# Performance work log

Hardware: AMD Instinct MI355X
Metric: run time of the kernel (lower is better)

Reference implementation:

```python
import jax, jax.numpy as jnp
import numpy as np

N_LAYERS = 2
K_NEIGHBOURS = 30  # graph_top_K keeps k_neighbours + 1 entries per row
EPS = 1e-12        # torch F.normalize eps


def setup_inputs() -> dict:
    key = jax.random.key(0)
    k1, k2 = jax.random.split(key)
    N, d = 8192, 512
    x = jax.random.normal(k1, (N, d), dtype=jnp.float32)
    W = jax.random.normal(k2, (N_LAYERS, d, d), dtype=jnp.float32) * 0.02
    b = jnp.zeros((N_LAYERS, d), dtype=jnp.float32)
    return {"x": x, "W": W, "b": b}


def reference(x, W, b):
    # MLP: interval_forward -- relu between layers, linear on last layer
    h = x
    for i in range(N_LAYERS - 1):
        h = jax.nn.relu(h @ W[i].T + b[i])
    h = h @ W[N_LAYERS - 1].T + b[N_LAYERS - 1]

    # F.normalize(h, dim=-1, p=2)
    norm = jnp.linalg.norm(h, axis=-1, keepdims=True)
    h = h / jnp.maximum(norm, EPS)

    # cal_similarity_graph: dense N x N cosine similarity
    sim = h @ h.T  # [N, N]

    # graph_top_K(sim, k+1): keep top-(k+1) values per row, zero elsewhere
    k = K_NEIGHBOURS + 1
    vals, idx = jax.lax.top_k(sim, k)  # [N, k]
    N = sim.shape[0]
    masked = jnp.zeros_like(sim).at[jnp.arange(N)[:, None], idx].set(vals)

    # apply_non_linearity(x, 'relu', slope, alpha) -> relu
    return jax.nn.relu(masked)
```

## Files before the change

### kernel.cpp

```cpp
#include <hip/hip_runtime.h>
#include <hip/hip_bf16.h>

typedef __attribute__((ext_vector_type(8))) short bf16x8;
typedef __attribute__((ext_vector_type(8))) unsigned short u16x8;
typedef __attribute__((ext_vector_type(4))) float f32x4;

__global__ __launch_bounds__(256)
void gemm_nt(const float* __restrict__ A, const float* __restrict__ B,
             const float* __restrict__ bias, float* __restrict__ C,
             int M, int N, int K, int do_relu)
{
    constexpr int KS = 16;
    constexpr int LDT = 132;
    __shared__ float As[KS * LDT];
    __shared__ float Bs[KS * LDT];

    const int t    = threadIdx.x;
    const int row0 = blockIdx.y * 128;
    const int col0 = blockIdx.x * 128;
    const int tm   = t & 15;
    const int tn   = t >> 4;
    const int lrow = t >> 2;
    const int lk   = (t & 3) << 2;

    const float* Ap0 = A + (size_t)(row0 + lrow)      * K + lk;
    const float* Ap1 = A + (size_t)(row0 + lrow + 64) * K + lk;
    const float* Bp0 = B + (size_t)(col0 + lrow)      * K + lk;
    const float* Bp1 = B + (size_t)(col0 + lrow + 64) * K + lk;

    float4 a0 = *(const float4*)(Ap0);
    float4 a1 = *(const float4*)(Ap1);
    float4 b0 = *(const float4*)(Bp0);
    float4 b1 = *(const float4*)(Bp1);

    float acc[8][8];
#pragma unroll
    for (int i = 0; i < 8; ++i)
#pragma unroll
        for (int j = 0; j < 8; ++j) acc[i][j] = 0.f;

    for (int k0 = 0; k0 < K; k0 += KS) {
        __syncthreads();
        As[(lk + 0) * LDT + lrow] = a0.x;
        As[(lk + 1) * LDT + lrow] = a0.y;
        As[(lk + 2) * LDT + lrow] = a0.z;
        As[(lk + 3) * LDT + lrow] = a0.w;
        As[(lk + 0) * LDT + lrow + 64] = a1.x;
        As[(lk + 1) * LDT + lrow + 64] = a1.y;
        As[(lk + 2) * LDT + lrow + 64] = a1.z;
        As[(lk + 3) * LDT + lrow + 64] = a1.w;
        Bs[(lk + 0) * LDT + lrow] = b0.x;
        Bs[(lk + 1) * LDT + lrow] = b0.y;
        Bs[(lk + 2) * LDT + lrow] = b0.z;
        Bs[(lk + 3) * LDT + lrow] = b0.w;
        Bs[(lk + 0) * LDT + lrow + 64] = b1.x;
        Bs[(lk + 1) * LDT + lrow + 64] = b1.y;
        Bs[(lk + 2) * LDT + lrow + 64] = b1.z;
        Bs[(lk + 3) * LDT + lrow + 64] = b1.w;
        __syncthreads();
        if (k0 + KS < K) {
            a0 = *(const float4*)(Ap0 + k0 + KS);
            a1 = *(const float4*)(Ap1 + k0 + KS);
            b0 = *(const float4*)(Bp0 + k0 + KS);
            b1 = *(const float4*)(Bp1 + k0 + KS);
        }
#pragma unroll
        for (int kk = 0; kk < KS; ++kk) {
            const float4 av0 = *(const float4*)&As[kk * LDT + 8 * tm];
            const float4 av1 = *(const float4*)&As[kk * LDT + 8 * tm + 4];
            const float4 bv0 = *(const float4*)&Bs[kk * LDT + 8 * tn];
            const float4 bv1 = *(const float4*)&Bs[kk * LDT + 8 * tn + 4];
            const float a[8] = {av0.x, av0.y, av0.z, av0.w, av1.x, av1.y, av1.z, av1.w};
            const float bb[8] = {bv0.x, bv0.y, bv0.z, bv0.w, bv1.x, bv1.y, bv1.z, bv1.w};
#pragma unroll
            for (int i = 0; i < 8; ++i)
#pragma unroll
                for (int j = 0; j < 8; ++j)
                    acc[i][j] += a[i] * bb[j];
        }
    }

#pragma unroll
    for (int i = 0; i < 8; ++i) {
        const int r = row0 + 8 * tm + i;
        float* Crow = C + (size_t)r * N + col0 + 8 * tn;
        float o[8];
#pragma unroll
        for (int j = 0; j < 8; ++j) o[j] = acc[i][j];
        if (bias) {
#pragma unroll
            for (int j = 0; j < 8; ++j) o[j] += bias[col0 + 8 * tn + j];
        }
        if (do_relu) {
#pragma unroll
            for (int j = 0; j < 8; ++j) o[j] = fmaxf(o[j], 0.f);
        }
        float4 o0 = {o[0], o[1], o[2], o[3]};
        float4 o1 = {o[4], o[5], o[6], o[7]};
        *(float4*)(Crow)     = o0;
        *(float4*)(Crow + 4) = o1;
    }
}

__global__ __launch_bounds__(128)
void rownorm_split(const float* __restrict__ in, unsigned short* __restrict__ Hhi,
                   unsigned short* __restrict__ Hmid, unsigned short* __restrict__ Hlo)
{
    __shared__ float s[2];
    const int r = blockIdx.x, t = threadIdx.x;
    const float4 v = ((const float4*)(in + (size_t)r * 512))[t];
    float ss = v.x * v.x + v.y * v.y + v.z * v.z + v.w * v.w;
#pragma unroll
    for (int off = 32; off; off >>= 1) ss += __shfl_down(ss, off);
    if ((t & 63) == 0) s[t >> 6] = ss;
    __syncthreads();
    const float den = fmaxf(sqrtf(s[0] + s[1]), 1e-12f);
    const float f[4] = {v.x / den, v.y / den, v.z / den, v.w / den};
    ushort4 uh, um, ul;
    unsigned short* ph = (unsigned short*)&uh;
    unsigned short* pm = (unsigned short*)&um;
    unsigned short* pl = (unsigned short*)&ul;
#pragma unroll
    for (int j = 0; j < 4; ++j) {
        const __hip_bfloat16 h = __float2bfloat16(f[j]);
        const float fh = __bfloat162float(h);
        const float r1 = f[j] - fh;
        const __hip_bfloat16 m = __float2bfloat16(r1);
        const float fm = __bfloat162float(m);
        const float r2 = r1 - fm;
        const __hip_bfloat16 l = __float2bfloat16(r2);
        ph[j] = *(const unsigned short*)&h;
        pm[j] = *(const unsigned short*)&m;
        pl[j] = *(const unsigned short*)&l;
    }
    const size_t o = (size_t)r * 512 + 4 * t;
    *(ushort4*)(Hhi  + o) = uh;
    *(ushort4*)(Hmid + o) = um;
    *(ushort4*)(Hlo  + o) = ul;
}

__global__ __launch_bounds__(256)
void gemm_sym_mfma(const unsigned short* __restrict__ Hhi,
                   const unsigned short* __restrict__ Hmid,
                   const unsigned short* __restrict__ Hlo,
                   float* __restrict__ C, int Nn)
{
    constexpr int K  = 512;
    constexpr int KC = 32;
    constexpr int LR = 40;
    __shared__ unsigned short lds[6 * 128 * LR];

    const int q = blockIdx.x;
    int ct = (int)((sqrtf(8.0f * (float)q + 1.0f) - 1.0f) * 0.5f);
    while ((ct + 1) * (ct + 2) / 2 <= q) ++ct;
    while (ct * (ct + 1) / 2 > q) --ct;
    const int rt = q - ct * (ct + 1) / 2;
    const int row0 = rt * 128;
    const int col0 = ct * 128;

    const int t    = threadIdx.x;
    const int lane = t & 63;
    const int wid  = t >> 6;
    const int wr   = (wid >> 1) * 64;
    const int wc   = (wid & 1) * 64;

    const int r  = t >> 1;
    const int kh = (t & 1) * 16;
    const unsigned short* srcs[6] = {
        Hhi  + (size_t)(row0 + r) * K, Hmid + (size_t)(row0 + r) * K, Hlo + (size_t)(row0 + r) * K,
        Hhi  + (size_t)(col0 + r) * K, Hmid + (size_t)(col0 + r) * K, Hlo + (size_t)(col0 + r) * K };

    u16x8 pf[12];
#pragma unroll
    for (int a = 0; a < 6; ++a) {
        pf[2 * a]     = *(const u16x8*)(srcs[a] + kh);
        pf[2 * a + 1] = *(const u16x8*)(srcs[a] + kh + 8);
    }

    f32x4 acc[4][4];
#pragma unroll
    for (int i = 0; i < 4; ++i)
#pragma unroll
        for (int j = 0; j < 4; ++j) acc[i][j] = (f32x4){0.f, 0.f, 0.f, 0.f};

    const int fro = (lane & 15) * LR + 8 * (lane >> 4);

    for (int k0 = 0; k0 < K; k0 += KC) {
        __syncthreads();
#pragma unroll
        for (int a = 0; a < 6; ++a) {
            *(u16x8*)&lds[a * 128 * LR + r * LR + kh]     = pf[2 * a];
            *(u16x8*)&lds[a * 128 * LR + r * LR + kh + 8] = pf[2 * a + 1];
        }
        __syncthreads();
        if (k0 + KC < K) {
#pragma unroll
            for (int a = 0; a < 6; ++a) {
                pf[2 * a]     = *(const u16x8*)(srcs[a] + k0 + KC + kh);
                pf[2 * a + 1] = *(const u16x8*)(srcs[a] + k0 + KC + kh + 8);
            }
        }
        bf16x8 af[3][4], bf[3][4];
#pragma unroll
        for (int p = 0; p < 3; ++p)
#pragma unroll
            for (int ti = 0; ti < 4; ++ti) {
                af[p][ti] = *(const bf16x8*)&lds[p * 128 * LR + (wr + ti * 16) * LR + fro];
                bf[p][ti] = *(const bf16x8*)&lds[(3 + p) * 128 * LR + (wc + ti * 16) * LR + fro];
            }
#pragma unroll
        for (int ti = 0; ti < 4; ++ti)
#pragma unroll
            for (int tj = 0; tj < 4; ++tj) {
                f32x4 c = acc[ti][tj];
                c = __builtin_amdgcn_mfma_f32_16x16x32_bf16(af[0][ti], bf[0][tj], c, 0, 0, 0);
                c = __builtin_amdgcn_mfma_f32_16x16x32_bf16(af[0][ti], bf[1][tj], c, 0, 0, 0);
                c = __builtin_amdgcn_mfma_f32_16x16x32_bf16(af[1][ti], bf[0][tj], c, 0, 0, 0);
                c = __builtin_amdgcn_mfma_f32_16x16x32_bf16(af[1][ti], bf[1][tj], c, 0, 0, 0);
                c = __builtin_amdgcn_mfma_f32_16x16x32_bf16(af[0][ti], bf[2][tj], c, 0, 0, 0);
                c = __builtin_amdgcn_mfma_f32_16x16x32_bf16(af[2][ti], bf[0][tj], c, 0, 0, 0);
                acc[ti][tj] = c;
            }
    }

    const int crow = (lane >> 4) * 4;
    const int ccol = lane & 15;
#pragma unroll
    for (int ti = 0; ti < 4; ++ti)
#pragma unroll
        for (int tj = 0; tj < 4; ++tj)
#pragma unroll
            for (int qq = 0; qq < 4; ++qq) {
                const int rr = row0 + wr + ti * 16 + crow + qq;
                const int cc = col0 + wc + tj * 16 + ccol;
                C[(size_t)rr * Nn + cc] = acc[ti][tj][qq];
            }
    if (ct != rt) {
#pragma unroll
        for (int ti = 0; ti < 4; ++ti)
#pragma unroll
            for (int tj = 0; tj < 4; ++tj)
#pragma unroll
                for (int qq = 0; qq < 4; ++qq) {
                    const int rr = row0 + wr + ti * 16 + crow + qq;
                    const int cc = col0 + wc + tj * 16 + ccol;
                    C[(size_t)cc * Nn + rr] = acc[ti][tj][qq];
                }
    }
}

__global__ __launch_bounds__(128)
void rownorm(const float* __restrict__ in, float* __restrict__ out)
{
    __shared__ float s[2];
    const int r = blockIdx.x, t = threadIdx.x;
    const float4 v = ((const float4*)(in + (size_t)r * 512))[t];
    float ss = v.x * v.x + v.y * v.y + v.z * v.z + v.w * v.w;
#pragma unroll
    for (int off = 32; off; off >>= 1) ss += __shfl_down(ss, off);
    if ((t & 63) == 0) s[t >> 6] = ss;
    __syncthreads();
    const float den = fmaxf(sqrtf(s[0] + s[1]), 1e-12f);
    float4 o;
    o.x = v.x / den; o.y = v.y / den; o.z = v.z / den; o.w = v.w / den;
    ((float4*)(out + (size_t)r * 512))[t] = o;
}

__global__ __launch_bounds__(256)
void gemm_syn(const float* __restrict__ H, float* __restrict__ C, int Nn, int K)
{
    constexpr int KS = 16;
    constexpr int LDT = 132;
    __shared__ float As[KS * LDT];
    __shared__ float Bs[KS * LDT];

    const int q = blockIdx.x;
    int ct = (int)((sqrtf(8.0f * (float)q + 1.0f) - 1.0f) * 0.5f);
    while ((ct + 1) * (ct + 2) / 2 <= q) ++ct;
    while (ct * (ct + 1) / 2 > q) --ct;
    const int rt = q - ct * (ct + 1) / 2;
    const int row0 = rt * 128;
    const int col0 = ct * 128;

    const int t    = threadIdx.x;
    const int tm   = t & 15;
    const int tn   = t >> 4;
    const int lrow = t >> 2;
    const int lk   = (t & 3) << 2;

    const float* Ap0 = H + (size_t)(row0 + lrow)      * K + lk;
    const float* Ap1 = H + (size_t)(row0 + lrow + 64) * K + lk;
    const float* Bp0 = H + (size_t)(col0 + lrow)      * K + lk;
    const float* Bp1 = H + (size_t)(col0 + lrow + 64) * K + lk;

    float4 a0 = *(const float4*)(Ap0);
    float4 a1 = *(const float4*)(Ap1);
    float4 b0 = *(const float4*)(Bp0);
    float4 b1 = *(const float4*)(Bp1);

    float acc[8][8];
#pragma unroll
    for (int i = 0; i < 8; ++i)
#pragma unroll
        for (int j = 0; j < 8; ++j) acc[i][j] = 0.f;

    for (int k0 = 0; k0 < K; k0 += KS) {
        __syncthreads();
        As[(lk + 0) * LDT + lrow] = a0.x;
        As[(lk + 1) * LDT + lrow] = a0.y;
        As[(lk + 2) * LDT + lrow] = a0.z;
        As[(lk + 3) * LDT + lrow] = a0.w;
        As[(lk + 0) * LDT + lrow + 64] = a1.x;
        As[(lk + 1) * LDT + lrow + 64] = a1.y;
        As[(lk + 2) * LDT + lrow + 64] = a1.z;
        As[(lk + 3) * LDT + lrow + 64] = a1.w;
        Bs[(lk + 0) * LDT + lrow] = b0.x;
        Bs[(lk + 1) * LDT + lrow] = b0.y;
        Bs[(lk + 2) * LDT + lrow] = b0.z;
        Bs[(lk + 3) * LDT + lrow] = b0.w;
        Bs[(lk + 0) * LDT + lrow + 64] = b1.x;
        Bs[(lk + 1) * LDT + lrow + 64] = b1.y;
        Bs[(lk + 2) * LDT + lrow + 64] = b1.z;
        Bs[(lk + 3) * LDT + lrow + 64] = b1.w;
        __syncthreads();
        if (k0 + KS < K) {
            a0 = *(const float4*)(Ap0 + k0 + KS);
            a1 = *(const float4*)(Ap1 + k0 + KS);
            b0 = *(const float4*)(Bp0 + k0 + KS);
            b1 = *(const float4*)(Bp1 + k0 + KS);
        }
#pragma unroll
        for (int kk = 0; kk < KS; ++kk) {
            const float4 av0 = *(const float4*)&As[kk * LDT + 4 * tm];
            const float4 av1 = *(const float4*)&As[kk * LDT + 4 * tm + 64];
            const float4 bv0 = *(const float4*)&Bs[kk * LDT + 4 * tn];
            const float4 bv1 = *(const float4*)&Bs[kk * LDT + 4 * tn + 64];
            const float a[8] = {av0.x, av0.y, av0.z, av0.w, av1.x, av1.y, av1.z, av1.w};
            const float bb[8] = {bv0.x, bv0.y, bv0.z, bv0.w, bv1.x, bv1.y, bv1.z, bv1.w};
#pragma unroll
            for (int i = 0; i < 8; ++i)
#pragma unroll
                for (int j = 0; j < 8; ++j)
                    acc[i][j] += a[i] * bb[j];
        }
    }

#pragma unroll
    for (int ih = 0; ih < 2; ++ih)
#pragma unroll
    for (int i2 = 0; i2 < 4; ++i2) {
        const int rr = row0 + ih * 64 + 4 * tm + i2;
        float* Crow = C + (size_t)rr * Nn + col0;
        const int ia = ih * 4 + i2;
        float4 o0 = {acc[ia][0], acc[ia][1], acc[ia][2], acc[ia][3]};
        float4 o1 = {acc[ia][4], acc[ia][5], acc[ia][6], acc[ia][7]};
        *(float4*)(Crow + 4 * tn)      = o0;
        *(float4*)(Crow + 64 + 4 * tn) = o1;
    }
    if (ct != rt) {
#pragma unroll
        for (int jh = 0; jh < 2; ++jh)
#pragma unroll
        for (int j2 = 0; j2 < 4; ++j2) {
            const int rr = col0 + jh * 64 + 4 * tn + j2;
            float* Crow = C + (size_t)rr * Nn + row0;
            const int ja = jh * 4 + j2;
            float4 o0 = {acc[0][ja], acc[1][ja], acc[2][ja], acc[3][ja]};
            float4 o1 = {acc[4][ja], acc[5][ja], acc[6][ja], acc[7][ja]};
            *(float4*)(Crow + 4 * tm)      = o0;
            *(float4*)(Crow + 64 + 4 * tm) = o1;
        }
    }
}

__device__ __forceinline__ unsigned monou(unsigned b)
{
    return (b & 0x80000000u) ? ~b : (b | 0x80000000u);
}
__device__ __forceinline__ float unmono(unsigned u)
{
    return __uint_as_float((u & 0x80000000u) ? (u ^ 0x80000000u) : ~u);
}

__global__ __launch_bounds__(256)
void topk_bits(float* __restrict__ sim)
{
    constexpr int NC = 8192;
    constexpr unsigned KSEL = 31;
    __shared__ unsigned wsum[2][4];
    __shared__ int tie_idx[256];
    __shared__ int tie_cnt, sh_thr;

    const int t = threadIdx.x;
    const int lane = t & 63;
    const int wid = t >> 6;
    float* row = sim + (size_t)blockIdx.x * NC;

    if (t == 0) tie_cnt = 0;

    unsigned k[8][4];
#pragma unroll
    for (int j = 0; j < 8; ++j) {
        const uint4 v = *(const uint4*)&row[4 * (t + 256 * j)];
        k[j][0] = monou(v.x); k[j][1] = monou(v.y);
        k[j][2] = monou(v.z); k[j][3] = monou(v.w);
    }

    unsigned X = 0u;
    for (int b = 31; b >= 0; --b) {
        const unsigned cand = X | (1u << b);
        unsigned c = 0;
#pragma unroll
        for (int j = 0; j < 8; ++j)
#pragma unroll
            for (int e = 0; e < 4; ++e)
                c += (k[j][e] >= cand) ? 1u : 0u;
#pragma unroll
        for (int off = 32; off; off >>= 1) c += __shfl_xor(c, off);
        if (lane == 0) wsum[b & 1][wid] = c;
        __syncthreads();
        const unsigned tot = wsum[b & 1][0] + wsum[b & 1][1]
                           + wsum[b & 1][2] + wsum[b & 1][3];
        if (tot >= KSEL) X = cand;
    }
    const unsigned uc = X;

    {
        unsigned c = 0;
#pragma unroll
        for (int j = 0; j < 8; ++j)
#pragma unroll
            for (int e = 0; e < 4; ++e)
                c += (k[j][e] > uc) ? 1u : 0u;
#pragma unroll
        for (int off = 32; off; off >>= 1) c += __shfl_xor(c, off);
        if (lane == 0) wsum[1][wid] = c;
        __syncthreads();
    }
    const int m = (int)(KSEL - (wsum[1][0] + wsum[1][1] + wsum[1][2] + wsum[1][3]));

#pragma unroll
    for (int j = 0; j < 8; ++j)
#pragma unroll
        for (int e = 0; e < 4; ++e)
            if (k[j][e] == uc) {
                const int p = atomicAdd(&tie_cnt, 1);
                if (p < 256) tie_idx[p] = 4 * (t + 256 * j) + e;
            }
    __syncthreads();
    if (t == 0) {
        int n = tie_cnt < 256 ? tie_cnt : 256;
        for (int a = 1; a < n; ++a) {
            const int key = tie_idx[a];
            int c = a - 1;
            while (c >= 0 && tie_idx[c] > key) { tie_idx[c + 1] = tie_idx[c]; --c; }
            tie_idx[c + 1] = key;
        }
        const int mm = (m <= n ? m : n);
        sh_thr = tie_idx[mm - 1];
    }
    __syncthreads();
    const int tie_thr = sh_thr;

#pragma unroll
    for (int j = 0; j < 8; ++j) {
        const int i0 = 4 * (t + 256 * j);
        float4 v;
        v.x = (k[j][0] > uc || (k[j][0] == uc && i0 + 0 <= tie_thr)) ? fmaxf(unmono(k[j][0]), 0.f) : 0.f;
        v.y = (k[j][1] > uc || (k[j][1] == uc && i0 + 1 <= tie_thr)) ? fmaxf(unmono(k[j][1]), 0.f) : 0.f;
        v.z = (k[j][2] > uc || (k[j][2] == uc && i0 + 2 <= tie_thr)) ? fmaxf(unmono(k[j][2]), 0.f) : 0.f;
        v.w = (k[j][3] > uc || (k[j][3] == uc && i0 + 3 <= tie_thr)) ? fmaxf(unmono(k[j][3]), 0.f) : 0.f;
        *(float4*)&row[i0] = v;
    }
}

extern "C" void kernel_launch(void* const* d_in, const int* in_sizes, int n_in,
                              void* d_out, int out_size, void* d_ws, size_t ws_size,
                              hipStream_t stream)
{
    const float* x = (const float*)d_in[0];
    const float* W = (const float*)d_in[1];
    const float* b = (const float*)d_in[2];
    float* out = (float*)d_out;

    const int N = 8192, D = 512;
    const int T = N / 128;

    float* h1 = out;
    float* h2 = out + (size_t)N * D;

    dim3 tb(256);
    gemm_nt<<<dim3(D / 128, N / 128), tb, 0, stream>>>(x,  W,                 b,     h1, N, D, D, 1);
    gemm_nt<<<dim3(D / 128, N / 128), tb, 0, stream>>>(h1, W + (size_t)D * D, b + D, h2, N, D, D, 0);

    const size_t split_bytes = (size_t)3 * N * D * sizeof(unsigned short);
    if (ws_size >= split_bytes) {
        unsigned short* Hhi  = (unsigned short*)d_ws;
        unsigned short* Hmid = Hhi  + (size_t)N * D;
        unsigned short* Hlo  = Hmid + (size_t)N * D;
        rownorm_split<<<N, 128, 0, stream>>>(h2, Hhi, Hmid, Hlo);
        gemm_sym_mfma<<<T * (T + 1) / 2, tb, 0, stream>>>(Hhi, Hmid, Hlo, out, N);
    } else {
        float* hn = (float*)d_ws;
        rownorm<<<N, 128, 0, stream>>>(h2, hn);
        gemm_syn<<<T * (T + 1) / 2, tb, 0, stream>>>(hn, out, N, D);
    }
    topk_bits<<<N, tb, 0, stream>>>(out);
}
```

Measured before the change: 758.3 us.

## Shrink MLP GEMM tiles, swizzle MFMA LDS layout, and remap symmetric tile order

The MLP GEMMs move from 128x128 to 128x64 output tiles, doubling the block count to 512 so more CUs are busy, with a conflict-free strided thread mapping. In the symmetric bf16-split MFMA GEMM, the padded LDS rows are replaced by an XOR-swizzled 64-byte row layout to avoid bank conflicts without padding. Block indices are also permuted in an interleaved order (q0&7)*260+(q0>>3), which spreads triangular tiles across the GPU. Smaller MLP tiles lower per-block reuse, and the remap assumes exactly 2080 blocks.

After: 753.9 us. About the same (-0.6%).

```diff
diff --git a/kernel.cpp b/kernel.cpp
--- a/kernel.cpp
+++ b/kernel.cpp
@@ -6,27 +6,294 @@
 typedef __attribute__((ext_vector_type(4))) float f32x4;
 
 __global__ __launch_bounds__(256)
-void gemm_nt(const float* __restrict__ A, const float* __restrict__ B,
-             const float* __restrict__ bias, float* __restrict__ C,
-             int M, int N, int K, int do_relu)
+void gemm_nt64(const float* __restrict__ A, const float* __restrict__ B,
+               const float* __restrict__ bias, float* __restrict__ C,
+               int M, int N, int K, int do_relu)
+{
+    constexpr int KS = 16;
+    constexpr int LDA = 132;
+    constexpr int LDB = 68;
+    __shared__ float As[KS * LDA];
+    __shared__ float Bs[KS * LDB];
+
+    const int t    = threadIdx.x;
+    const int row0 = blockIdx.y * 128;
+    const int col0 = blockIdx.x * 64;
+    const int tm   = t & 15;
+    const int tn   = t >> 4;
+
+    const int arow = t >> 1;
+    const int ak   = (t & 1) * 8;
+    const int brow = t >> 2;
+    const int bk   = (t & 3) * 4;
+
+    const float* Ap = A + (size_t)(row0 + arow) * K + ak;
+    const float* Bp = B + (size_t)(col0 + brow) * K + bk;
+
+    float4 a0 = *(const float4*)(Ap);
+    float4 a1 = *(const float4*)(Ap + 4);
+    float4 b0 = *(const float4*)(Bp);
+
+    float acc[8][4];
+#pragma unroll
+    for (int i = 0; i < 8; ++i)
+#pragma unroll
+        for (int j = 0; j < 4; ++j) acc[i][j] = 0.f;
+
+    for (int k0 = 0; k0 < K; k0 += KS) {
+        __syncthreads();
+        As[(ak + 0) * LDA + arow] = a0.x;
+        As[(ak + 1) * LDA + arow] = a0.y;
+        As[(ak + 2) * LDA + arow] = a0.z;
+        As[(ak + 3) * LDA + arow] = a0.w;
+        As[(ak + 4) * LDA + arow] = a1.x;
+        As[(ak + 5) * LDA + arow] = a1.y;
+        As[(ak + 6) * LDA + arow] = a1.z;
+        As[(ak + 7) * LDA + arow] = a1.w;
+        Bs[(bk + 0) * LDB + brow] = b0.x;
+        Bs[(bk + 1) * LDB + brow] = b0.y;
+        Bs[(bk + 2) * LDB + brow] = b0.z;
+        Bs[(bk + 3) * LDB + brow] = b0.w;
+        __syncthreads();
+        if (k0 + KS < K) {
+            a0 = *(const float4*)(Ap + k0 + KS);
+            a1 = *(const float4*)(Ap + k0 + KS + 4);
+            b0 = *(const float4*)(Bp + k0 + KS);
+        }
+#pragma unroll
+        for (int kk = 0; kk < KS; ++kk) {
+            const float4 av0 = *(const float4*)&As[kk * LDA + 4 * tm];
+            const float4 av1 = *(const float4*)&As[kk * LDA + 64 + 4 * tm];
+            const float4 bv  = *(const float4*)&Bs[kk * LDB + 4 * tn];
+            const float a[8] = {av0.x, av0.y, av0.z, av0.w, av1.x, av1.y, av1.z, av1.w};
+            const float bb[4] = {bv.x, bv.y, bv.z, bv.w};
+#pragma unroll
+            for (int i = 0; i < 8; ++i)
+#pragma unroll
+                for (int j = 0; j < 4; ++j)
+                    acc[i][j] += a[i] * bb[j];
+        }
+    }
+
+#pragma unroll
+    for (int ih = 0; ih < 2; ++ih)
+#pragma unroll
+    for (int i2 = 0; i2 < 4; ++i2) {
+        const int r  = row0 + ih * 64 + 4 * tm + i2;
+        const int ia = ih * 4 + i2;
+        float o[4];
+#pragma unroll
+        for (int j = 0; j < 4; ++j) o[j] = acc[ia][j];
+        if (bias) {
+#pragma unroll
+            for (int j = 0; j < 4; ++j) o[j] += bias[col0 + 4 * tn + j];
+        }
+        if (do_relu) {
+#pragma unroll
+            for (int j = 0; j < 4; ++j) o[j] = fmaxf(o[j], 0.f);
+        }
+        float4 ov = {o[0], o[1], o[2], o[3]};
+        *(float4*)(C + (size_t)r * N + col0 + 4 * tn) = ov;
+    }
+}
+
+__global__ __launch_bounds__(128)
+void rownorm_split(const float* __restrict__ in, unsigned short* __restrict__ Hhi,
+                   unsigned short* __restrict__ Hmid, unsigned short* __restrict__ Hlo)
+{
+    __shared__ float s[2];
+    const int r = blockIdx.x, t = threadIdx.x;
+    const float4 v = ((const float4*)(in + (size_t)r * 512))[t];
+    float ss = v.x * v.x + v.y * v.y + v.z * v.z + v.w * v.w;
+#pragma unroll
+    for (int off = 32; off; off >>= 1) ss += __shfl_down(ss, off);
+    if ((t & 63) == 0) s[t >> 6] = ss;
+    __syncthreads();
+    const float den = fmaxf(sqrtf(s[0] + s[1]), 1e-12f);
+    const float f[4] = {v.x / den, v.y / den, v.z / den, v.w / den};
+    ushort4 uh, um, ul;
+    unsigned short* ph = (unsigned short*)&uh;
+    unsigned short* pm = (unsigned short*)&um;
+    unsigned short* pl = (unsigned short*)&ul;
+#pragma unroll
+    for (int j = 0; j < 4; ++j) {
+        const __hip_bfloat16 h = __float2bfloat16(f[j]);
+        const float fh = __bfloat162float(h);
+        const float r1 = f[j] - fh;
+        const __hip_bfloat16 m = __float2bfloat16(r1);
+        const float fm = __bfloat162float(m);
+        const float r2 = r1 - fm;
+        const __hip_bfloat16 l = __float2bfloat16(r2);
+        ph[j] = *(const unsigned short*)&h;
+        pm[j] = *(const unsigned short*)&m;
+        pl[j] = *(const unsigned short*)&l;
+    }
+    const size_t o = (size_t)r * 512 + 4 * t;
+    *(ushort4*)(Hhi  + o) = uh;
+    *(ushort4*)(Hmid + o) = um;
+    *(ushort4*)(Hlo  + o) = ul;
+}
+
+__global__ __launch_bounds__(256)
+void gemm_sym_mfma(const unsigned short* __restrict__ Hhi,
+                   const unsigned short* __restrict__ Hmid,
+                   const unsigned short* __restrict__ Hlo,
+                   float* __restrict__ C, int Nn)
+{
+    constexpr int K  = 512;
+    constexpr int KC = 32;
+    __shared__ unsigned short lds[6 * 128 * 32];
+
+    const int q0 = blockIdx.x;
+    const int q  = (q0 & 7) * 260 + (q0 >> 3);
+    int ct = (int)((sqrtf(8.0f * (float)q + 1.0f) - 1.0f) * 0.5f);
+    while ((ct + 1) * (ct + 2) / 2 <= q) ++ct;
+    while (ct * (ct + 1) / 2 > q) --ct;
+    const int rt = q - ct * (ct + 1) / 2;
+    const int row0 = rt * 128;
+    const int col0 = ct * 128;
+
+    const int t    = threadIdx.x;
+    const int lane = t & 63;
+    const int wid  = t >> 6;
+    const int wr   = (wid >> 1) * 64;
+    const int wc   = (wid & 1) * 64;
+
+    const int r   = t >> 1;
+    const int kh  = (t & 1) * 16;
+    const int wb  = r * 64 + kh * 2;
+    const int swW = ((r & 7) << 4);
+    const unsigned short* srcs[6] = {
+        Hhi  + (size_t)(row0 + r) * K, Hmid + (size_t)(row0 + r) * K, Hlo + (size_t)(row0 + r) * K,
+        Hhi  + (size_t)(col0 + r) * K, Hmid + (size_t)(col0 + r) * K, Hlo + (size_t)(col0 + r) * K };
+
+    u16x8 pf[12];
+#pragma unroll
+    for (int a = 0; a < 6; ++a) {
+        pf[2 * a]     = *(const u16x8*)(srcs[a] + kh);
+        pf[2 * a + 1] = *(const u16x8*)(srcs[a] + kh + 8);
+    }
+
+    f32x4 acc[4][4];
+#pragma unroll
+    for (int i = 0; i < 4; ++i)
+#pragma unroll
+        for (int j = 0; j < 4; ++j) acc[i][j] = (f32x4){0.f, 0.f, 0.f, 0.f};
+
+    const int g16 = (lane >> 4) << 4;
+    const int swR = ((lane & 7) << 4);
+    char* ldsb = (char*)lds;
+
+    for (int k0 = 0; k0 < K; k0 += KC) {
+        __syncthreads();
+#pragma unroll
+        for (int a = 0; a < 6; ++a) {
+            const int base = a * 8192 + wb;
+            *(u16x8*)(ldsb + ((base)      ^ swW)) = pf[2 * a];
+            *(u16x8*)(ldsb + ((base + 16) ^ swW)) = pf[2 * a + 1];
+        }
+        __syncthreads();
+        if (k0 + KC < K) {
+#pragma unroll
+            for (int a = 0; a < 6; ++a) {
+                pf[2 * a]     = *(const u16x8*)(srcs[a] + k0 + KC + kh);
+                pf[2 * a + 1] = *(const u16x8*)(srcs[a] + k0 + KC + kh + 8);
+            }
+        }
+        bf16x8 af[3][4], bf[3][4];
+#pragma unroll
+        for (int p = 0; p < 3; ++p)
+#pragma unroll
+            for (int ti = 0; ti < 4; ++ti) {
+                const int rA = wr + ti * 16 + (lane & 15);
+                const int rB = wc + ti * 16 + (lane & 15);
+                af[p][ti] = *(const bf16x8*)(ldsb + ((p * 8192 + rA * 64 + g16) ^ swR));
+                bf[p][ti] = *(const bf16x8*)(ldsb + (((3 + p) * 8192 + rB * 64 + g16) ^ swR));
+            }
+#pragma unroll
+        for (int ti = 0; ti < 4; ++ti)
+#pragma unroll
+            for (int tj = 0; tj < 4; ++tj) {
+                f32x4 c = acc[ti][tj];
+                c = __builtin_amdgcn_mfma_f32_16x16x32_bf16(af[0][ti], bf[0][tj], c, 0, 0, 0);
+                c = __builtin_amdgcn_mfma_f32_16x16x32_bf16(af[0][ti], bf[1][tj], c, 0, 0, 0);
+                c = __builtin_amdgcn_mfma_f32_16x16x32_bf16(af[1][ti], bf[0][tj], c, 0, 0, 0);
+                c = __builtin_amdgcn_mfma_f32_16x16x32_bf16(af[1][ti], bf[1][tj], c, 0, 0, 0);
+                c = __builtin_amdgcn_mfma_f32_16x16x32_bf16(af[0][ti], bf[2][tj], c, 0, 0, 0);
+                c = __builtin_amdgcn_mfma_f32_16x16x32_bf16(af[2][ti], bf[0][tj], c, 0, 0, 0);
+                acc[ti][tj] = c;
+            }
+    }
+
+    const int crow = (lane >> 4) * 4;
+    const int ccol = lane & 15;
+#pragma unroll
+    for (int ti = 0; ti < 4; ++ti)
+#pragma unroll
+        for (int tj = 0; tj < 4; ++tj)
+#pragma unroll
+            for (int qq = 0; qq < 4; ++qq) {
+                const int rr = row0 + wr + ti * 16 + crow + qq;
+                const int cc = col0 + wc + tj * 16 + ccol;
+                C[(size_t)rr * Nn + cc] = acc[ti][tj][qq];
+            }
+    if (ct != rt) {
+#pragma unroll
+        for (int ti = 0; ti < 4; ++ti)
+#pragma unroll
+            for (int tj = 0; tj < 4; ++tj)
+#pragma unroll
+                for (int qq = 0; qq < 4; ++qq) {
+                    const int rr = row0 + wr + ti * 16 + crow + qq;
+                    const int cc = col0 + wc + tj * 16 + ccol;
+                    C[(size_t)cc * Nn + rr] = acc[ti][tj][qq];
+                }
+    }
+}
+
+__global__ __launch_bounds__(128)
+void rownorm(const float* __restrict__ in, float* __restrict__ out)
+{
+    __shared__ float s[2];
+    const int r = blockIdx.x, t = threadIdx.x;
+    const float4 v = ((const float4*)(in + (size_t)r * 512))[t];
+    float ss = v.x * v.x + v.y * v.y + v.z * v.z + v.w * v.w;
+#pragma unroll
+    for (int off = 32; off; off >>= 1) ss += __shfl_down(ss, off);
+    if ((t & 63) == 0) s[t >> 6] = ss;
+    __syncthreads();
+    const float den = fmaxf(sqrtf(s[0] + s[1]), 1e-12f);
+    float4 o;
+    o.x = v.x / den; o.y = v.y / den; o.z = v.z / den; o.w = v.w / den;
+    ((float4*)(out + (size_t)r * 512))[t] = o;
+}
+
+__global__ __launch_bounds__(256)
+void gemm_syn(const float* __restrict__ H, float* __restrict__ C, int Nn, int K)
 {
     constexpr int KS = 16;
     constexpr int LDT = 132;
     __shared__ float As[KS * LDT];
     __shared__ float Bs[KS * LDT];
 
+    const int q = blockIdx.x;
+    int ct = (int)((sqrtf(8.0f * (float)q + 1.0f) - 1.0f) * 0.5f);
+    while ((ct + 1) * (ct + 2) / 2 <= q) ++ct;
+    while (ct * (ct + 1) / 2 > q) --ct;
+    const int rt = q - ct * (ct + 1) / 2;
+    const int row0 = rt * 128;
+    const int col0 = ct * 128;
+
     const int t    = threadIdx.x;
-    const int row0 = blockIdx.y * 128;
-    const int col0 = blockIdx.x * 128;
     const int tm   = t & 15;
     const int tn   = t >> 4;
     const int lrow = t >> 2;
     const int lk   = (t & 3) << 2;
 
-    const float* Ap0 = A + (size_t)(row0 + lrow)      * K + lk;
-    const float* Ap1 = A + (size_t)(row0 + lrow + 64) * K + lk;
-    const float* Bp0 = B + (size_t)(col0 + lrow)      * K + lk;
-    const float* Bp1 = B + (size_t)(col0 + lrow + 64) * K + lk;
+    const float* Ap0 = H + (size_t)(row0 + lrow)      * K + lk;
+    const float* Ap1 = H + (size_t)(row0 + lrow + 64) * K + lk;
+    const float* Bp0 = H + (size_t)(col0 + lrow)      * K + lk;
+    const float* Bp1 = H + (size_t)(col0 + lrow + 64) * K + lk;
 
     float4 a0 = *(const float4*)(Ap0);
     float4 a1 = *(const float4*)(Ap1);
@@ -66,271 +333,6 @@
         }
 #pragma unroll
         for (int kk = 0; kk < KS; ++kk) {
-            const float4 av0 = *(const float4*)&As[kk * LDT + 8 * tm];
-            const float4 av1 = *(const float4*)&As[kk * LDT + 8 * tm + 4];
-            const float4 bv0 = *(const float4*)&Bs[kk * LDT + 8 * tn];
-            const float4 bv1 = *(const float4*)&Bs[kk * LDT + 8 * tn + 4];
-            const float a[8] = {av0.x, av0.y, av0.z, av0.w, av1.x, av1.y, av1.z, av1.w};
-            const float bb[8] = {bv0.x, bv0.y, bv0.z, bv0.w, bv1.x, bv1.y, bv1.z, bv1.w};
-#pragma unroll
-            for (int i = 0; i < 8; ++i)
-#pragma unroll
-                for (int j = 0; j < 8; ++j)
-                    acc[i][j] += a[i] * bb[j];
-        }
-    }
-
-#pragma unroll
-    for (int i = 0; i < 8; ++i) {
-        const int r = row0 + 8 * tm + i;
-        float* Crow = C + (size_t)r * N + col0 + 8 * tn;
-        float o[8];
-#pragma unroll
-        for (int j = 0; j < 8; ++j) o[j] = acc[i][j];
-        if (bias) {
-#pragma unroll
-            for (int j = 0; j < 8; ++j) o[j] += bias[col0 + 8 * tn + j];
-        }
-        if (do_relu) {
-#pragma unroll
-            for (int j = 0; j < 8; ++j) o[j] = fmaxf(o[j], 0.f);
-        }
-        float4 o0 = {o[0], o[1], o[2], o[3]};
-        float4 o1 = {o[4], o[5], o[6], o[7]};
-        *(float4*)(Crow)     = o0;
-        *(float4*)(Crow + 4) = o1;
-    }
-}
-
-__global__ __launch_bounds__(128)
-void rownorm_split(const float* __restrict__ in, unsigned short* __restrict__ Hhi,
-                   unsigned short* __restrict__ Hmid, unsigned short* __restrict__ Hlo)
-{
-    __shared__ float s[2];
-    const int r = blockIdx.x, t = threadIdx.x;
-    const float4 v = ((const float4*)(in + (size_t)r * 512))[t];
-    float ss = v.x * v.x + v.y * v.y + v.z * v.z + v.w * v.w;
-#pragma unroll
-    for (int off = 32; off; off >>= 1) ss += __shfl_down(ss, off);
-    if ((t & 63) == 0) s[t >> 6] = ss;
-    __syncthreads();
-    const float den = fmaxf(sqrtf(s[0] + s[1]), 1e-12f);
-    const float f[4] = {v.x / den, v.y / den, v.z / den, v.w / den};
-    ushort4 uh, um, ul;
-    unsigned short* ph = (unsigned short*)&uh;
-    unsigned short* pm = (unsigned short*)&um;
-    unsigned short* pl = (unsigned short*)&ul;
-#pragma unroll
-    for (int j = 0; j < 4; ++j) {
-        const __hip_bfloat16 h = __float2bfloat16(f[j]);
-        const float fh = __bfloat162float(h);
-        const float r1 = f[j] - fh;
-        const __hip_bfloat16 m = __float2bfloat16(r1);
-        const float fm = __bfloat162float(m);
-        const float r2 = r1 - fm;
-        const __hip_bfloat16 l = __float2bfloat16(r2);
-        ph[j] = *(const unsigned short*)&h;
-        pm[j] = *(const unsigned short*)&m;
-        pl[j] = *(const unsigned short*)&l;
-    }
-    const size_t o = (size_t)r * 512 + 4 * t;
-    *(ushort4*)(Hhi  + o) = uh;
-    *(ushort4*)(Hmid + o) = um;
-    *(ushort4*)(Hlo  + o) = ul;
-}
-
-__global__ __launch_bounds__(256)
-void gemm_sym_mfma(const unsigned short* __restrict__ Hhi,
-                   const unsigned short* __restrict__ Hmid,
-                   const unsigned short* __restrict__ Hlo,
-                   float* __restrict__ C, int Nn)
-{
-    constexpr int K  = 512;
-    constexpr int KC = 32;
-    constexpr int LR = 40;
-    __shared__ unsigned short lds[6 * 128 * LR];
-
-    const int q = blockIdx.x;
-    int ct = (int)((sqrtf(8.0f * (float)q + 1.0f) - 1.0f) * 0.5f);
-    while ((ct + 1) * (ct + 2) / 2 <= q) ++ct;
-    while (ct * (ct + 1) / 2 > q) --ct;
-    const int rt = q - ct * (ct + 1) / 2;
-    const int row0 = rt * 128;
-    const int col0 = ct * 128;
-
-    const int t    = threadIdx.x;
-    const int lane = t & 63;
-    const int wid  = t >> 6;
-    const int wr   = (wid >> 1) * 64;
-    const int wc   = (wid & 1) * 64;
-
-    const int r  = t >> 1;
-    const int kh = (t & 1) * 16;
-    const unsigned short* srcs[6] = {
-        Hhi  + (size_t)(row0 + r) * K, Hmid + (size_t)(row0 + r) * K, Hlo + (size_t)(row0 + r) * K,
-        Hhi  + (size_t)(col0 + r) * K, Hmid + (size_t)(col0 + r) * K, Hlo + (size_t)(col0 + r) * K };
-
-    u16x8 pf[12];
-#pragma unroll
-    for (int a = 0; a < 6; ++a) {
-        pf[2 * a]     = *(const u16x8*)(srcs[a] + kh);
-        pf[2 * a + 1] = *(const u16x8*)(srcs[a] + kh + 8);
-    }
-
-    f32x4 acc[4][4];
-#pragma unroll
-    for (int i = 0; i < 4; ++i)
-#pragma unroll
-        for (int j = 0; j < 4; ++j) acc[i][j] = (f32x4){0.f, 0.f, 0.f, 0.f};
-
-    const int fro = (lane & 15) * LR + 8 * (lane >> 4);
-
-    for (int k0 = 0; k0 < K; k0 += KC) {
-        __syncthreads();
-#pragma unroll
-        for (int a = 0; a < 6; ++a) {
-            *(u16x8*)&lds[a * 128 * LR + r * LR + kh]     = pf[2 * a];
-            *(u16x8*)&lds[a * 128 * LR + r * LR + kh + 8] = pf[2 * a + 1];
-        }
-        __syncthreads();
-        if (k0 + KC < K) {
-#pragma unroll
-            for (int a = 0; a < 6; ++a) {
-                pf[2 * a]     = *(const u16x8*)(srcs[a] + k0 + KC + kh);
-                pf[2 * a + 1] = *(const u16x8*)(srcs[a] + k0 + KC + kh + 8);
-            }
-        }
-        bf16x8 af[3][4], bf[3][4];
-#pragma unroll
-        for (int p = 0; p < 3; ++p)
-#pragma unroll
-            for (int ti = 0; ti < 4; ++ti) {
-                af[p][ti] = *(const bf16x8*)&lds[p * 128 * LR + (wr + ti * 16) * LR + fro];
-                bf[p][ti] = *(const bf16x8*)&lds[(3 + p) * 128 * LR + (wc + ti * 16) * LR + fro];
-            }
-#pragma unroll
-        for (int ti = 0; ti < 4; ++ti)
-#pragma unroll
-            for (int tj = 0; tj < 4; ++tj) {
-                f32x4 c = acc[ti][tj];
-                c = __builtin_amdgcn_mfma_f32_16x16x32_bf16(af[0][ti], bf[0][tj], c, 0, 0, 0);
-                c = __builtin_amdgcn_mfma_f32_16x16x32_bf16(af[0][ti], bf[1][tj], c, 0, 0, 0);
-                c = __builtin_amdgcn_mfma_f32_16x16x32_bf16(af[1][ti], bf[0][tj], c, 0, 0, 0);
-                c = __builtin_amdgcn_mfma_f32_16x16x32_bf16(af[1][ti], bf[1][tj], c, 0, 0, 0);
-                c = __builtin_amdgcn_mfma_f32_16x16x32_bf16(af[0][ti], bf[2][tj], c, 0, 0, 0);
-                c = __builtin_amdgcn_mfma_f32_16x16x32_bf16(af[2][ti], bf[0][tj], c, 0, 0, 0);
-                acc[ti][tj] = c;
-            }
-    }
-
-    const int crow = (lane >> 4) * 4;
-    const int ccol = lane & 15;
-#pragma unroll
-    for (int ti = 0; ti < 4; ++ti)
-#pragma unroll
-        for (int tj = 0; tj < 4; ++tj)
-#pragma unroll
-            for (int qq = 0; qq < 4; ++qq) {
-                const int rr = row0 + wr + ti * 16 + crow + qq;
-                const int cc = col0 + wc + tj * 16 + ccol;
-                C[(size_t)rr * Nn + cc] = acc[ti][tj][qq];
-            }
-    if (ct != rt) {
-#pragma unroll
-        for (int ti = 0; ti < 4; ++ti)
-#pragma unroll
-            for (int tj = 0; tj < 4; ++tj)
-#pragma unroll
-                for (int qq = 0; qq < 4; ++qq) {
-                    const int rr = row0 + wr + ti * 16 + crow + qq;
-                    const int cc = col0 + wc + tj * 16 + ccol;
-                    C[(size_t)cc * Nn + rr] = acc[ti][tj][qq];
-                }
-    }
-}
-
-__global__ __launch_bounds__(128)
-void rownorm(const float* __restrict__ in, float* __restrict__ out)
-{
-    __shared__ float s[2];
-    const int r = blockIdx.x, t = threadIdx.x;
-    const float4 v = ((const float4*)(in + (size_t)r * 512))[t];
-    float ss = v.x * v.x + v.y * v.y + v.z * v.z + v.w * v.w;
-#pragma unroll
-    for (int off = 32; off; off >>= 1) ss += __shfl_down(ss, off);
-    if ((t & 63) == 0) s[t >> 6] = ss;
-    __syncthreads();
-    const float den = fmaxf(sqrtf(s[0] + s[1]), 1e-12f);
-    float4 o;
-    o.x = v.x / den; o.y = v.y / den; o.z = v.z / den; o.w = v.w / den;
-    ((float4*)(out + (size_t)r * 512))[t] = o;
-}
-
-__global__ __launch_bounds__(256)
-void gemm_syn(const float* __restrict__ H, float* __restrict__ C, int Nn, int K)
-{
-    constexpr int KS = 16;
-    constexpr int LDT = 132;
-    __shared__ float As[KS * LDT];
-    __shared__ float Bs[KS * LDT];
-
-    const int q = blockIdx.x;
-    int ct = (int)((sqrtf(8.0f * (float)q + 1.0f) - 1.0f) * 0.5f);
-    while ((ct + 1) * (ct + 2) / 2 <= q) ++ct;
-    while (ct * (ct + 1) / 2 > q) --ct;
-    const int rt = q - ct * (ct + 1) / 2;
-    const int row0 = rt * 128;
-    const int col0 = ct * 128;
-
-    const int t    = threadIdx.x;
-    const int tm   = t & 15;
-    const int tn   = t >> 4;
-    const int lrow = t >> 2;
-    const int lk   = (t & 3) << 2;
-
-    const float* Ap0 = H + (size_t)(row0 + lrow)      * K + lk;
-    const float* Ap1 = H + (size_t)(row0 + lrow + 64) * K + lk;
-    const float* Bp0 = H + (size_t)(col0 + lrow)      * K + lk;
-    const float* Bp1 = H + (size_t)(col0 + lrow + 64) * K + lk;
-
-    float4 a0 = *(const float4*)(Ap0);
-    float4 a1 = *(const float4*)(Ap1);
-    float4 b0 = *(const float4*)(Bp0);
-    float4 b1 = *(const float4*)(Bp1);
-
-    float acc[8][8];
-#pragma unroll
-    for (int i = 0; i < 8; ++i)
-#pragma unroll
-        for (int j = 0; j < 8; ++j) acc[i][j] = 0.f;
-
-    for (int k0 = 0; k0 < K; k0 += KS) {
-        __syncthreads();
-        As[(lk + 0) * LDT + lrow] = a0.x;
-        As[(lk + 1) * LDT + lrow] = a0.y;
-        As[(lk + 2) * LDT + lrow] = a0.z;
-        As[(lk + 3) * LDT + lrow] = a0.w;
-        As[(lk + 0) * LDT + lrow + 64] = a1.x;
-        As[(lk + 1) * LDT + lrow + 64] = a1.y;
-        As[(lk + 2) * LDT + lrow + 64] = a1.z;
-        As[(lk + 3) * LDT + lrow + 64] = a1.w;
-        Bs[(lk + 0) * LDT + lrow] = b0.x;
-        Bs[(lk + 1) * LDT + lrow] = b0.y;
-        Bs[(lk + 2) * LDT + lrow] = b0.z;
-        Bs[(lk + 3) * LDT + lrow] = b0.w;
-        Bs[(lk + 0) * LDT + lrow + 64] = b1.x;
-        Bs[(lk + 1) * LDT + lrow + 64] = b1.y;
-        Bs[(lk + 2) * LDT + lrow + 64] = b1.z;
-        Bs[(lk + 3) * LDT + lrow + 64] = b1.w;
-        __syncthreads();
-        if (k0 + KS < K) {
-            a0 = *(const float4*)(Ap0 + k0 + KS);
-            a1 = *(const float4*)(Ap1 + k0 + KS);
-            b0 = *(const float4*)(Bp0 + k0 + KS);
-            b1 = *(const float4*)(Bp1 + k0 + KS);
-        }
-#pragma unroll
-        for (int kk = 0; kk < KS; ++kk) {
             const float4 av0 = *(const float4*)&As[kk * LDT + 4 * tm];
             const float4 av1 = *(const float4*)&As[kk * LDT + 4 * tm + 64];
             const float4 bv0 = *(const float4*)&Bs[kk * LDT + 4 * tn];
@@ -490,8 +492,8 @@
     float* h2 = out + (size_t)N * D;
 
     dim3 tb(256);
-    gemm_nt<<<dim3(D / 128, N / 128), tb, 0, stream>>>(x,  W,                 b,     h1, N, D, D, 1);
-    gemm_nt<<<dim3(D / 128, N / 128), tb, 0, stream>>>(h1, W + (size_t)D * D, b + D, h2, N, D, D, 0);
+    gemm_nt64<<<dim3(D / 64, N / 128), tb, 0, stream>>>(x,  W,                 b,     h1, N, D, D, 1);
+    gemm_nt64<<<dim3(D / 64, N / 128), tb, 0, stream>>>(h1, W + (size_t)D * D, b + D, h2, N, D, D, 0);
 
     const size_t split_bytes = (size_t)3 * N * D * sizeof(unsigned short);
     if (ws_size >= split_bytes) {
```
